# Kernel optimization log

Measured on AMD Instinct MI355X. Metric: run time of the kernel, lower is better.

Reference implementation:

```python
import jax, jax.numpy as jnp
import numpy as np

CONF_TH = 0.6      # confidence_threshold
IOU_TH = 0.45      # iou_threshold
MAX_WH = 4096.0    # class offset for class-aware NMS (agnostic=False)
TOP_K = 1024       # fixed candidate cap (analog of max_nms, jit-static)
MAX_DET = 300      # max detections per image
NC = 80
AGNOSTIC = False


def setup_inputs() -> dict:
    key = jax.random.key(0)
    k1, k2 = jax.random.split(key)
    prediction = jax.random.uniform(k1, (16, 25200, 85), dtype=jnp.float32)
    logits = jax.random.uniform(k2, (16, 25200, 80), dtype=jnp.float32)
    return {"prediction": prediction, "logits": logits}


def xywh2xyxy(b):
    cx, cy, w, h = b[:, 0], b[:, 1], b[:, 2], b[:, 3]
    return jnp.stack([cx - w * 0.5, cy - h * 0.5, cx + w * 0.5, cy + h * 0.5], axis=-1)


def box_iou(a, b):
    # a: [K,4], b: [K,4] in xyxy -> [K,K] IoU
    area_a = (a[:, 2] - a[:, 0]) * (a[:, 3] - a[:, 1])
    area_b = (b[:, 2] - b[:, 0]) * (b[:, 3] - b[:, 1])
    lt = jnp.maximum(a[:, None, :2], b[None, :, :2])
    rb = jnp.minimum(a[:, None, 2:], b[None, :, 2:])
    wh = jnp.clip(rb - lt, 0.0)
    inter = wh[..., 0] * wh[..., 1]
    return inter / (area_a[:, None] + area_b[None, :] - inter + 1e-9)


def _greedy_keep(iou, valid):
    # iou: [K,K] on score-descending boxes; valid: [K] bool
    K = iou.shape[0]
    ar = jnp.arange(K)

    def step(suppressed, i):
        keep_i = valid[i] & ~suppressed[i]
        suppressed = suppressed | (keep_i & (iou[i] > IOU_TH) & (ar > i))
        return suppressed, keep_i

    _, keep = jax.lax.scan(step, jnp.zeros((K,), dtype=bool), ar)
    return keep


def _nms_image(pred, logit):
    # pred: [N, 5+nc], logit: [N, nc]
    obj = pred[:, 4]
    cls_scores = pred[:, 5:] * obj[:, None]          # x[:,5:] *= x[:,4:5]
    conf = jnp.max(cls_scores, axis=-1)              # best-class confidence
    cls = jnp.argmax(cls_scores, axis=-1)
    valid = (obj > CONF_TH) & (conf > CONF_TH)       # xc gate + conf gate
    box = xywh2xyxy(pred[:, :4])

    score = jnp.where(valid, conf, -1.0)
    top_scores, idx = jax.lax.top_k(score, TOP_K)    # descending-score candidates
    box_k = box[idx]                                  # [K,4] original boxes
    cls_k = cls[idx]
    logit_k = logit[idx]
    valid_k = top_scores > CONF_TH

    # class-aware offset (agnostic=False) for NMS only
    off = 0.0 if AGNOSTIC else MAX_WH
    nms_boxes = box_k + cls_k[:, None].astype(box_k.dtype) * off

    iou = box_iou(nms_boxes, nms_boxes)
    keep = _greedy_keep(iou, valid_k)

    kept_score = jnp.where(keep, top_scores, -1.0)
    sel_score, sel = jax.lax.top_k(kept_score, MAX_DET)
    out_valid = sel_score > CONF_TH

    det = jnp.concatenate(
        [box_k[sel], top_scores[sel][:, None], cls_k[sel][:, None].astype(jnp.float32)],
        axis=1,
    )  # [max_det, 6] = [xyxy, conf, cls]
    det = jnp.where(out_valid[:, None], det, 0.0)
    logits_out = jnp.where(out_valid[:, None], logit_k[sel], 0.0)  # [max_det, nc]
    return det, out_valid, logits_out


def reference(prediction, logits):
    det, valid, logits_out = jax.vmap(_nms_image)(prediction, logits)
    return det, valid, logits_out
```

## Files before the change

kernel.cpp:

```cpp
#include <hip/hip_runtime.h>
#include <stdint.h>

#define CONF_THR 0.6f
#define IOU_THR  0.45f
#define MAX_WH_F 4096.0f
#define TOPK     1024
#define MAX_DET  300
#define NCLS     80
#define ROW      85
#define APB      128
#define RING     16

typedef unsigned int u32;
typedef unsigned long long u64;

__device__ __forceinline__ u32 f2s(float f) {
    u32 b = __float_as_uint(f);
    return b ^ ((u32)((int)b >> 31) | 0x80000000u);
}
__device__ __forceinline__ float s2f(u32 k) {
    u32 b = (k & 0x80000000u) ? (k ^ 0x80000000u) : ~k;
    return __uint_as_float(b);
}

__global__ __launch_bounds__(256) void k_score(const float* __restrict__ pred,
        u32* __restrict__ key, u32* __restrict__ cls, int NA) {
#pragma clang fp contract(off)
    int img = blockIdx.y;
    int a0 = blockIdx.x * APB;
    int count = min(APB, NA - a0);
    if (count <= 0) return;
    size_t baseoff = ((size_t)img * NA + a0) * ROW;
    const float* base = pred + baseoff;
    __shared__ __align__(16) float tile[APB * ROW];
    int nfloat = count * ROW;
    if ((baseoff & 3) == 0) {
        int nvec = nfloat >> 2;
        const float4* b4 = (const float4*)base;
        float4* t4 = (float4*)tile;
        for (int i = threadIdx.x; i < nvec; i += blockDim.x) t4[i] = b4[i];
        for (int i = (nvec << 2) + threadIdx.x; i < nfloat; i += blockDim.x)
            tile[i] = base[i];
    } else {
        for (int i = threadIdx.x; i < nfloat; i += blockDim.x) tile[i] = base[i];
    }
    __syncthreads();
    int t = threadIdx.x;
    if (t < count) {
        const float* r = tile + t * ROW;
        float obj = r[4];
        float maxv = -1.0f; int cl = 0;
        for (int j = 0; j < NCLS; ++j) {
            float v = r[5 + j] * obj;
            if (v > maxv) { maxv = v; cl = j; }
        }
        bool valid = (obj > CONF_THR) && (maxv > CONF_THR);
        float score = valid ? maxv : -1.0f;
        size_t g = (size_t)img * NA + a0 + t;
        key[g] = f2s(score);
        cls[g] = (u32)cl;
    }
}

__global__ __launch_bounds__(1024) void k_topk(const u32* __restrict__ key,
        const float* __restrict__ pred, const u32* __restrict__ cls,
        u32* __restrict__ top_idx, float* __restrict__ top_score,
        float* __restrict__ boxk, float* __restrict__ nmsbox,
        float* __restrict__ clsf, int NA) {
#pragma clang fp contract(off)
    int img = blockIdx.x;
    const u32* kb = key + (size_t)img * NA;
    __shared__ u32 whist[16 * 256];
    __shared__ u32 hfin[256];
    __shared__ int sh_d;
    __shared__ u32 sh_t;
    __shared__ u32 gcnt;
    __shared__ u64 skey[TOPK];
    int tid = threadIdx.x;
    int wid = tid >> 6, lane = tid & 63;
    u64 lanemask = (1ull << lane) - 1ull;
    u32 prefix = 0, target = TOPK;
    for (int level = 0; level < 4; ++level) {
        int shift = 24 - 8 * level;
        for (int i = tid; i < 16 * 256; i += 1024) whist[i] = 0;
        __syncthreads();
        for (int idx0 = 0; idx0 < NA; idx0 += 1024) {
            int idx = idx0 + tid;
            bool inb = idx < NA;
            u32 k = inb ? kb[idx] : 0u;
            bool in = inb && ((level == 0) || ((k >> (shift + 8)) == prefix));
            u32 d = (k >> shift) & 0xFFu;
            if (level == 0) {
                u64 peers = __ballot(in);
#pragma unroll
                for (int bit = 0; bit < 8; ++bit) {
                    u64 bb = __ballot((d >> bit) & 1u);
                    peers &= ((d >> bit) & 1u) ? bb : ~bb;
                }
                if (in) {
                    int leader = (int)(__ffsll((long long)peers) - 1);
                    if (lane == leader)
                        atomicAdd(&whist[(wid << 8) | d], (u32)__popcll(peers));
                }
            } else {
                if (in) atomicAdd(&whist[(wid << 8) | d], 1u);
            }
        }
        __syncthreads();
        if (tid < 256) {
            u32 s = 0;
#pragma unroll
            for (int w = 0; w < 16; ++w) s += whist[(w << 8) | tid];
            hfin[tid] = s;
        }
        __syncthreads();
        if (tid < 64) {
            u32 h0 = hfin[4 * tid], h1 = hfin[4 * tid + 1];
            u32 h2 = hfin[4 * tid + 2], h3 = hfin[4 * tid + 3];
            u32 s = h0 + h1 + h2 + h3;
            u32 t = s;
#pragma unroll
            for (int off = 1; off < 64; off <<= 1) {
                u32 o = (u32)__shfl_down((int)t, off);
                if (tid + off < 64) t += o;
            }
            u32 S0 = t, S1 = t - h0, S2 = S1 - h1, S3 = S2 - h2, S4 = t - s;
            u32 tg = target;
            if (S0 >= tg && S1 < tg) { sh_d = 4 * tid;     sh_t = tg - S1; }
            if (S1 >= tg && S2 < tg) { sh_d = 4 * tid + 1; sh_t = tg - S2; }
            if (S2 >= tg && S3 < tg) { sh_d = 4 * tid + 2; sh_t = tg - S3; }
            if (S3 >= tg && S4 < tg) { sh_d = 4 * tid + 3; sh_t = tg - S4; }
        }
        __syncthreads();
        prefix = (prefix << 8) | (u32)sh_d;
        target = sh_t;
    }
    u32 cutv = prefix;
    u32 R = target;
    u32 T = hfin[cutv & 0xFFu];
    if (tid == 0) gcnt = 0;
    __syncthreads();
    bool takeTies = (T == R);
    for (int c0 = 0; c0 < NA; c0 += 1024) {
        int idx = c0 + tid;
        bool inb = idx < NA;
        u32 k = inb ? kb[idx] : 0u;
        bool put = inb && ((k > cutv) || (takeTies && k == cutv));
        u64 ball = __ballot(put);
        if (ball) {
            int leader = (int)(__ffsll((long long)ball) - 1);
            u32 base = 0;
            if (lane == leader) base = atomicAdd(&gcnt, (u32)__popcll(ball));
            base = __shfl(base, leader);
            if (put)
                skey[base + (u32)__popcll(ball & lanemask)] =
                    ((u64)k << 32) | (u64)(u32)(NA - 1 - idx);
        }
    }
    __syncthreads();
    if (!takeTies) {
        u32 G = gcnt;
        if (tid < 64) {
            u32 cnt = 0;
            for (int c0 = 0; c0 < NA; c0 += 64) {
                int idx = c0 + tid;
                bool ist = (idx < NA) && (kb[idx] == cutv);
                u64 ball = __ballot(ist);
                u32 rank = cnt + (u32)__popcll(ball & lanemask);
                if (ist && rank < R)
                    skey[G + rank] = ((u64)cutv << 32) | (u64)(u32)(NA - 1 - idx);
                cnt += (u32)__popcll(ball);
                if (cnt >= R) break;
            }
        }
        __syncthreads();
    }
    int jprev = 0;
    for (int k2 = 2; k2 <= TOPK; k2 <<= 1) {
        for (int j = k2 >> 1; j > 0; j >>= 1) {
            if (j >= 64 || jprev >= 64) __syncthreads();
            int i = tid, ixj = i ^ j;
            if (ixj > i) {
                u64 a = skey[i], b = skey[ixj];
                bool desc = ((i & k2) == 0);
                if ((a < b) == desc) { skey[i] = b; skey[ixj] = a; }
            }
            jprev = j;
        }
    }
    __syncthreads();
    u64 kk = skey[tid];
    u32 aidx = (u32)(NA - 1) - (u32)(kk & 0xFFFFFFFFull);
    float sc = s2f((u32)(kk >> 32));
    int g = img * TOPK + tid;
    top_idx[g] = aidx;
    top_score[g] = sc;
    const float* r = pred + ((size_t)img * NA + aidx) * ROW;
    float cx = r[0], cy = r[1], w4 = r[2], h4 = r[3];
    float hw = w4 * 0.5f, hh = h4 * 0.5f;
    float x1 = cx - hw, y1 = cy - hh, x2 = cx + hw, y2 = cy + hh;
    u32 c = cls[(size_t)img * NA + aidx];
    float off = (float)c * MAX_WH_F;
    boxk[g * 4 + 0] = x1; boxk[g * 4 + 1] = y1;
    boxk[g * 4 + 2] = x2; boxk[g * 4 + 3] = y2;
    nmsbox[g * 4 + 0] = x1 + off; nmsbox[g * 4 + 1] = y1 + off;
    nmsbox[g * 4 + 2] = x2 + off; nmsbox[g * 4 + 3] = y2 + off;
    clsf[g] = (float)c;
}

__global__ __launch_bounds__(1024) void k_mask(const float* __restrict__ nmsbox,
        u64* __restrict__ mask) {
#pragma clang fp contract(off)
    int img = blockIdx.y;
    __shared__ float bx[TOPK + 32], by[TOPK + 32], bX[TOPK + 32], bY[TOPK + 32], ar[TOPK + 32];
    int tid = threadIdx.x;
    {
        const float4* nb = (const float4*)(nmsbox + (size_t)img * TOPK * 4);
        float4 b = nb[tid];
        int pi = tid + (tid >> 5);
        bx[pi] = b.x; by[pi] = b.y; bX[pi] = b.z; bY[pi] = b.w;
        ar[pi] = (b.z - b.x) * (b.w - b.y);
    }
    __syncthreads();
    int i = blockIdx.x * 64 + (tid >> 4);
    int w = tid & 15;
    int pi = i + (i >> 5);
    float ax = bx[pi], ay = by[pi], aX = bX[pi], aY = bY[pi], aa = ar[pi];
    u64 bits = 0;
    for (int jj = 0; jj < 64; ++jj) {
        int j = (w << 6) + jj;
        if (j > i) {
            int pj = j + (j >> 5);
            float ltx = fmaxf(ax, bx[pj]);
            float lty = fmaxf(ay, by[pj]);
            float rbx = fminf(aX, bX[pj]);
            float rby = fminf(aY, bY[pj]);
            float ww = fmaxf(rbx - ltx, 0.0f);
            float hh = fmaxf(rby - lty, 0.0f);
            float inter = ww * hh;
            float denom = ((aa + ar[pj]) - inter) + 1e-9f;
            float iou = inter / denom;
            if (iou > IOU_THR) bits |= (1ull << jj);
        }
    }
    mask[((size_t)img * TOPK + i) * 16 + w] = bits;
}

__global__ __launch_bounds__(1024) void k_nms(const u64* __restrict__ mask,
        const float* __restrict__ top_score,
        u32* __restrict__ sel, u32* __restrict__ selcnt, u32* __restrict__ dummy) {
    __shared__ u32 s_nvalid;
    __shared__ u64 keepw[16];
    int img = blockIdx.x;
    int tid = threadIdx.x;
    int lane = tid & 63;
    if (tid == 0) s_nvalid = 0;
    if (tid < 16) keepw[tid] = 0;
    __syncthreads();
    {
        float s = top_score[img * TOPK + tid];
        u64 b = __ballot(s > CONF_THR);
        if (lane == 0) atomicAdd(&s_nvalid, (u32)__popcll(b));
    }
    __syncthreads();
    const u64* mrow = mask + (size_t)img * TOPK * 16;
    if (tid >= 64) {
        const uint4* m16 = (const uint4*)mrow;
        u32 acc = 0;
        for (int i = tid - 64; i < 8192; i += 960) {
            uint4 v = m16[i];
            acc ^= v.x ^ v.y ^ v.z ^ v.w;
        }
        if (acc == 0xDEADBEEFu) *dummy = acc;
        return;
    }
    int nvalid = (int)s_nvalid;
    bool ld = lane < 16;
    u64 rem = 0;
    u64 pf[RING];
#pragma unroll
    for (int k = 0; k < RING; ++k)
        pf[k] = ld ? mrow[(size_t)k * 16 + lane] : 0ull;
    int nblk = (nvalid + 63) >> 6;
    int kept_total = 0;
    for (int blk = 0; blk < nblk; ++blk) {
        u64 kw = 0;
        int base = blk << 6;
#pragma unroll 16
        for (int t = 0; t < 64; ++t) {
            int i = base + t;
            u64 roww = pf[i & (RING - 1)];
            int nx = i + RING;
            pf[i & (RING - 1)] = (ld && nx < TOPK) ? mrow[(size_t)nx * 16 + lane] : 0ull;
            bool notsup = (lane == (i >> 6)) && !((rem >> (i & 63)) & 1ull);
            if (__ballot(notsup) != 0ull) {
                rem |= roww;
                kw |= (1ull << t);
            }
        }
        int over = nvalid - base;
        if (over < 64) kw &= (over <= 0) ? 0ull : ((1ull << over) - 1ull);
        if (lane == 0) keepw[blk] = kw;
        kept_total += (int)__popcll(kw);
        if (kept_total >= MAX_DET) break;
    }
    if (lane < 16) {
        u64 kw = keepw[lane];
        u32 rank = 0;
        for (int m = 0; m < 16; ++m)
            if (m < lane) rank += (u32)__popcll(keepw[m]);
        while (kw) {
            int b = (int)__ffsll((long long)kw) - 1;
            if (rank < MAX_DET) sel[img * MAX_DET + rank] = (u32)((lane << 6) + b);
            ++rank;
            kw &= kw - 1;
        }
    }
    if (lane == 0) selcnt[img] = (u32)min(kept_total, MAX_DET);
}

__global__ void k_out(const float* __restrict__ logits,
        const u32* __restrict__ top_idx, const float* __restrict__ top_score,
        const float* __restrict__ boxk, const float* __restrict__ clsf,
        const u32* __restrict__ sel, const u32* __restrict__ selcnt,
        float* __restrict__ out, int NA, int B) {
    int img = blockIdx.y;
    int t = blockIdx.x;
    int tid = threadIdx.x;
    u32 K = selcnt[img];
    size_t detoff = ((size_t)img * MAX_DET + t) * 6;
    size_t voff = (size_t)B * MAX_DET * 6 + (size_t)img * MAX_DET + t;
    size_t loff = (size_t)B * MAX_DET * 7 + ((size_t)img * MAX_DET + t) * NCLS;
    if ((u32)t < K) {
        int slot = (int)sel[img * MAX_DET + t];
        int g = img * TOPK + slot;
        u32 aidx = top_idx[g];
        if (tid < NCLS)      out[loff + tid] = logits[((size_t)img * NA + aidx) * NCLS + tid];
        else if (tid < 84)   out[detoff + (tid - 80)] = boxk[(size_t)g * 4 + (tid - 80)];
        else if (tid == 84)  out[detoff + 4] = top_score[g];
        else if (tid == 85)  out[detoff + 5] = clsf[g];
        else if (tid == 86)  out[voff] = 1.0f;
    } else {
        if (tid < NCLS)      out[loff + tid] = 0.0f;
        else if (tid < 86)   out[detoff + (tid - 80)] = 0.0f;
        else if (tid == 86)  out[voff] = 0.0f;
    }
}

extern "C" void kernel_launch(void* const* d_in, const int* in_sizes, int n_in,
                              void* d_out, int out_size, void* d_ws, size_t ws_size,
                              hipStream_t stream) {
    const float* pred = (const float*)d_in[0];
    const float* logits = (const float*)d_in[1];
    float* out = (float*)d_out;
    const int B = out_size / (MAX_DET * (6 + 1 + NCLS));
    const int NA = in_sizes[0] / (B * ROW);

    char* p = (char*)d_ws;
    auto alloc = [&](size_t bytes) -> void* {
        void* r = (void*)p;
        p += (bytes + 255) & ~(size_t)255;
        return r;
    };
    u32* key       = (u32*)alloc((size_t)B * NA * 4);
    u32* cls       = (u32*)alloc((size_t)B * NA * 4);
    u32* top_idx   = (u32*)alloc((size_t)B * TOPK * 4);
    float* top_scr = (float*)alloc((size_t)B * TOPK * 4);
    float* boxk    = (float*)alloc((size_t)B * TOPK * 16);
    float* nmsbox  = (float*)alloc((size_t)B * TOPK * 16);
    float* clsf    = (float*)alloc((size_t)B * TOPK * 4);
    u64* mask      = (u64*)alloc((size_t)B * TOPK * 16 * 8);
    u32* sel       = (u32*)alloc((size_t)B * MAX_DET * 4);
    u32* selcnt    = (u32*)alloc((size_t)(B + 1) * 4);
    u32* dummy     = selcnt + B;

    k_score<<<dim3((NA + APB - 1) / APB, B), 256, 0, stream>>>(pred, key, cls, NA);
    k_topk<<<dim3(B), 1024, 0, stream>>>(key, pred, cls, top_idx, top_scr,
                                         boxk, nmsbox, clsf, NA);
    k_mask<<<dim3(TOPK / 64, B), 1024, 0, stream>>>(nmsbox, mask);
    k_nms<<<dim3(B), 1024, 0, stream>>>(mask, top_scr, sel, selcnt, dummy);
    k_out<<<dim3(MAX_DET, B), 128, 0, stream>>>(logits, top_idx, top_scr, boxk, clsf,
                                                sel, selcnt, out, NA, B);
}
```

Baseline: 368.1 us.

## Cache 16-bit keys in LDS, compact candidates for top-k, fuse output into NMS

```diff
diff --git a/kernel.cpp b/kernel.cpp
--- a/kernel.cpp
+++ b/kernel.cpp
@@ -10,6 +10,7 @@
 #define ROW      85
 #define APB      128
 #define RING     16
+#define CAND2    1024
 
 typedef unsigned int u32;
 typedef unsigned long long u64;
@@ -21,6 +22,39 @@
 __device__ __forceinline__ float s2f(u32 k) {
     u32 b = (k & 0x80000000u) ? (k ^ 0x80000000u) : ~k;
     return __uint_as_float(b);
+}
+
+__device__ __forceinline__ void hist_add(u32* hist, u32 d, bool in, int lane) {
+    u64 peers = __ballot(in);
+#pragma unroll
+    for (int bit = 0; bit < 8; ++bit) {
+        u64 bb = __ballot((d >> bit) & 1u);
+        peers &= ((d >> bit) & 1u) ? bb : ~bb;
+    }
+    if (in) {
+        int leader = (int)(__ffsll((long long)peers) - 1);
+        if (lane == leader) atomicAdd(&hist[d], (u32)__popcll(peers));
+    }
+}
+
+__device__ __forceinline__ void suffix_select(const u32* hist, int tid, u32 target,
+                                              int* sh_d, u32* sh_t) {
+    if (tid < 64) {
+        u32 h0 = hist[4 * tid], h1 = hist[4 * tid + 1];
+        u32 h2 = hist[4 * tid + 2], h3 = hist[4 * tid + 3];
+        u32 s = h0 + h1 + h2 + h3;
+        u32 t = s;
+#pragma unroll
+        for (int off = 1; off < 64; off <<= 1) {
+            u32 o = (u32)__shfl_down((int)t, off);
+            if (tid + off < 64) t += o;
+        }
+        u32 S0 = t, S1 = t - h0, S2 = S1 - h1, S3 = S2 - h2, S4 = t - s;
+        if (S0 >= target && S1 < target) { *sh_d = 4 * tid;     *sh_t = target - S1; }
+        if (S1 >= target && S2 < target) { *sh_d = 4 * tid + 1; *sh_t = target - S2; }
+        if (S2 >= target && S3 < target) { *sh_d = 4 * tid + 2; *sh_t = target - S3; }
+        if (S3 >= target && S4 < target) { *sh_d = 4 * tid + 3; *sh_t = target - S4; }
+    }
 }
 
 __global__ __launch_bounds__(256) void k_score(const float* __restrict__ pred,
@@ -70,74 +104,94 @@
 #pragma clang fp contract(off)
     int img = blockIdx.x;
     const u32* kb = key + (size_t)img * NA;
-    __shared__ u32 whist[16 * 256];
-    __shared__ u32 hfin[256];
+    __shared__ u32 hist[256];
     __shared__ int sh_d;
     __shared__ u32 sh_t;
-    __shared__ u32 gcnt;
-    __shared__ u64 skey[TOPK];
+    __shared__ u32 gcnt, ccnt;
+    struct ShA { unsigned short key16[25216]; u32 cand2[CAND2]; };
+    union ShU { ShA a; u64 skey[TOPK]; };
+    __shared__ ShU sh;
     int tid = threadIdx.x;
-    int wid = tid >> 6, lane = tid & 63;
+    int lane = tid & 63;
     u64 lanemask = (1ull << lane) - 1ull;
-    u32 prefix = 0, target = TOPK;
-    for (int level = 0; level < 4; ++level) {
+    u32 target = TOPK;
+
+    if (tid < 256) hist[tid] = 0;
+    __syncthreads();
+    for (int c0 = 0; c0 < NA; c0 += 1024) {
+        int idx = c0 + tid;
+        bool inb = idx < NA;
+        u32 k = inb ? kb[idx] : 0u;
+        if (inb) sh.a.key16[idx] = (unsigned short)(k >> 16);
+        hist_add(hist, k >> 24, inb, lane);
+    }
+    __syncthreads();
+    suffix_select(hist, tid, target, &sh_d, &sh_t);
+    __syncthreads();
+    u32 d0 = (u32)sh_d; target = sh_t;
+
+    if (tid < 256) hist[tid] = 0;
+    __syncthreads();
+    for (int c0 = 0; c0 < NA; c0 += 1024) {
+        int idx = c0 + tid;
+        bool inb = idx < NA;
+        u32 v = inb ? (u32)sh.a.key16[idx] : 0u;
+        bool in = inb && ((v >> 8) == d0);
+        hist_add(hist, v & 0xFFu, in, lane);
+    }
+    __syncthreads();
+    suffix_select(hist, tid, target, &sh_d, &sh_t);
+    __syncthreads();
+    u32 prefix = (d0 << 8) | (u32)sh_d;
+    target = sh_t;
+
+    if (tid == 0) ccnt = 0;
+    __syncthreads();
+    for (int c0 = 0; c0 < NA; c0 += 1024) {
+        int idx = c0 + tid;
+        bool inb = idx < NA;
+        u32 k = inb ? kb[idx] : 0u;
+        bool put = inb && ((k >> 16) == prefix);
+        u64 ball = __ballot(put);
+        if (ball) {
+            int leader = (int)(__ffsll((long long)ball) - 1);
+            u32 base = 0;
+            if (lane == leader) base = atomicAdd(&ccnt, (u32)__popcll(ball));
+            base = __shfl(base, leader);
+            u32 pos = base + (u32)__popcll(ball & lanemask);
+            if (put && pos < CAND2) sh.a.cand2[pos] = k;
+        }
+    }
+    __syncthreads();
+    u32 nc = ccnt;
+
+    for (int level = 2; level < 4; ++level) {
         int shift = 24 - 8 * level;
-        for (int i = tid; i < 16 * 256; i += 1024) whist[i] = 0;
+        if (tid < 256) hist[tid] = 0;
         __syncthreads();
-        for (int idx0 = 0; idx0 < NA; idx0 += 1024) {
-            int idx = idx0 + tid;
-            bool inb = idx < NA;
-            u32 k = inb ? kb[idx] : 0u;
-            bool in = inb && ((level == 0) || ((k >> (shift + 8)) == prefix));
-            u32 d = (k >> shift) & 0xFFu;
-            if (level == 0) {
-                u64 peers = __ballot(in);
-#pragma unroll
-                for (int bit = 0; bit < 8; ++bit) {
-                    u64 bb = __ballot((d >> bit) & 1u);
-                    peers &= ((d >> bit) & 1u) ? bb : ~bb;
-                }
-                if (in) {
-                    int leader = (int)(__ffsll((long long)peers) - 1);
-                    if (lane == leader)
-                        atomicAdd(&whist[(wid << 8) | d], (u32)__popcll(peers));
-                }
-            } else {
-                if (in) atomicAdd(&whist[(wid << 8) | d], 1u);
+        if (nc <= CAND2) {
+            u32 k = (tid < (int)nc) ? sh.a.cand2[tid] : 0u;
+            bool in = (tid < (int)nc) &&
+                      ((level == 2) || ((k >> (shift + 8)) == prefix));
+            hist_add(hist, (k >> shift) & 0xFFu, in, lane);
+        } else {
+            for (int c0 = 0; c0 < NA; c0 += 1024) {
+                int idx = c0 + tid;
+                bool inb = idx < NA;
+                u32 k = inb ? kb[idx] : 0u;
+                bool in = inb && ((k >> (shift + 8)) == prefix);
+                hist_add(hist, (k >> shift) & 0xFFu, in, lane);
             }
         }
         __syncthreads();
-        if (tid < 256) {
-            u32 s = 0;
-#pragma unroll
-            for (int w = 0; w < 16; ++w) s += whist[(w << 8) | tid];
-            hfin[tid] = s;
-        }
-        __syncthreads();
-        if (tid < 64) {
-            u32 h0 = hfin[4 * tid], h1 = hfin[4 * tid + 1];
-            u32 h2 = hfin[4 * tid + 2], h3 = hfin[4 * tid + 3];
-            u32 s = h0 + h1 + h2 + h3;
-            u32 t = s;
-#pragma unroll
-            for (int off = 1; off < 64; off <<= 1) {
-                u32 o = (u32)__shfl_down((int)t, off);
-                if (tid + off < 64) t += o;
-            }
-            u32 S0 = t, S1 = t - h0, S2 = S1 - h1, S3 = S2 - h2, S4 = t - s;
-            u32 tg = target;
-            if (S0 >= tg && S1 < tg) { sh_d = 4 * tid;     sh_t = tg - S1; }
-            if (S1 >= tg && S2 < tg) { sh_d = 4 * tid + 1; sh_t = tg - S2; }
-            if (S2 >= tg && S3 < tg) { sh_d = 4 * tid + 2; sh_t = tg - S3; }
-            if (S3 >= tg && S4 < tg) { sh_d = 4 * tid + 3; sh_t = tg - S4; }
-        }
+        suffix_select(hist, tid, target, &sh_d, &sh_t);
         __syncthreads();
         prefix = (prefix << 8) | (u32)sh_d;
         target = sh_t;
     }
     u32 cutv = prefix;
     u32 R = target;
-    u32 T = hfin[cutv & 0xFFu];
+    u32 T = hist[cutv & 0xFFu];
     if (tid == 0) gcnt = 0;
     __syncthreads();
     bool takeTies = (T == R);
@@ -153,7 +207,7 @@
             if (lane == leader) base = atomicAdd(&gcnt, (u32)__popcll(ball));
             base = __shfl(base, leader);
             if (put)
-                skey[base + (u32)__popcll(ball & lanemask)] =
+                sh.skey[base + (u32)__popcll(ball & lanemask)] =
                     ((u64)k << 32) | (u64)(u32)(NA - 1 - idx);
         }
     }
@@ -168,7 +222,7 @@
                 u64 ball = __ballot(ist);
                 u32 rank = cnt + (u32)__popcll(ball & lanemask);
                 if (ist && rank < R)
-                    skey[G + rank] = ((u64)cutv << 32) | (u64)(u32)(NA - 1 - idx);
+                    sh.skey[G + rank] = ((u64)cutv << 32) | (u64)(u32)(NA - 1 - idx);
                 cnt += (u32)__popcll(ball);
                 if (cnt >= R) break;
             }
@@ -181,15 +235,15 @@
             if (j >= 64 || jprev >= 64) __syncthreads();
             int i = tid, ixj = i ^ j;
             if (ixj > i) {
-                u64 a = skey[i], b = skey[ixj];
+                u64 a = sh.skey[i], b = sh.skey[ixj];
                 bool desc = ((i & k2) == 0);
-                if ((a < b) == desc) { skey[i] = b; skey[ixj] = a; }
+                if ((a < b) == desc) { sh.skey[i] = b; sh.skey[ixj] = a; }
             }
             jprev = j;
         }
     }
     __syncthreads();
-    u64 kk = skey[tid];
+    u64 kk = sh.skey[tid];
     u32 aidx = (u32)(NA - 1) - (u32)(kk & 0xFFFFFFFFull);
     float sc = s2f((u32)(kk >> 32));
     int g = img * TOPK + tid;
@@ -247,12 +301,17 @@
 }
 
 __global__ __launch_bounds__(1024) void k_nms(const u64* __restrict__ mask,
-        const float* __restrict__ top_score,
-        u32* __restrict__ sel, u32* __restrict__ selcnt, u32* __restrict__ dummy) {
+        const float* __restrict__ top_score, const u32* __restrict__ top_idx,
+        const float* __restrict__ boxk, const float* __restrict__ clsf,
+        const float* __restrict__ logits, float* __restrict__ out,
+        u32* __restrict__ dummy, int NA, int B) {
     __shared__ u32 s_nvalid;
     __shared__ u64 keepw[16];
+    __shared__ u32 s_sel[MAX_DET];
+    __shared__ u32 s_cnt;
     int img = blockIdx.x;
     int tid = threadIdx.x;
+    int wid = tid >> 6;
     int lane = tid & 63;
     if (tid == 0) s_nvalid = 0;
     if (tid < 16) keepw[tid] = 0;
@@ -272,78 +331,69 @@
             acc ^= v.x ^ v.y ^ v.z ^ v.w;
         }
         if (acc == 0xDEADBEEFu) *dummy = acc;
-        return;
-    }
-    int nvalid = (int)s_nvalid;
-    bool ld = lane < 16;
-    u64 rem = 0;
-    u64 pf[RING];
+    } else {
+        int nvalid = (int)s_nvalid;
+        bool ld = lane < 16;
+        u64 rem = 0;
+        u64 pf[RING];
 #pragma unroll
-    for (int k = 0; k < RING; ++k)
-        pf[k] = ld ? mrow[(size_t)k * 16 + lane] : 0ull;
-    int nblk = (nvalid + 63) >> 6;
-    int kept_total = 0;
-    for (int blk = 0; blk < nblk; ++blk) {
-        u64 kw = 0;
-        int base = blk << 6;
+        for (int k = 0; k < RING; ++k)
+            pf[k] = ld ? mrow[(size_t)k * 16 + lane] : 0ull;
+        int nblk = (nvalid + 63) >> 6;
+        int kept_total = 0;
+        for (int blk = 0; blk < nblk; ++blk) {
+            u64 kw = 0;
+            int base = blk << 6;
 #pragma unroll 16
-        for (int t = 0; t < 64; ++t) {
-            int i = base + t;
-            u64 roww = pf[i & (RING - 1)];
-            int nx = i + RING;
-            pf[i & (RING - 1)] = (ld && nx < TOPK) ? mrow[(size_t)nx * 16 + lane] : 0ull;
-            bool notsup = (lane == (i >> 6)) && !((rem >> (i & 63)) & 1ull);
-            if (__ballot(notsup) != 0ull) {
-                rem |= roww;
-                kw |= (1ull << t);
+            for (int t = 0; t < 64; ++t) {
+                int i = base + t;
+                u64 roww = pf[i & (RING - 1)];
+                int nx = i + RING;
+                pf[i & (RING - 1)] = (ld && nx < TOPK) ? mrow[(size_t)nx * 16 + lane] : 0ull;
+                bool notsup = (lane == (i >> 6)) && !((rem >> (i & 63)) & 1ull);
+                if (__ballot(notsup) != 0ull) {
+                    rem |= roww;
+                    kw |= (1ull << t);
+                }
             }
-        }
-        int over = nvalid - base;
-        if (over < 64) kw &= (over <= 0) ? 0ull : ((1ull << over) - 1ull);
-        if (lane == 0) keepw[blk] = kw;
-        kept_total += (int)__popcll(kw);
-        if (kept_total >= MAX_DET) break;
-    }
-    if (lane < 16) {
-        u64 kw = keepw[lane];
-        u32 rank = 0;
-        for (int m = 0; m < 16; ++m)
-            if (m < lane) rank += (u32)__popcll(keepw[m]);
-        while (kw) {
-            int b = (int)__ffsll((long long)kw) - 1;
-            if (rank < MAX_DET) sel[img * MAX_DET + rank] = (u32)((lane << 6) + b);
-            ++rank;
-            kw &= kw - 1;
-        }
-    }
-    if (lane == 0) selcnt[img] = (u32)min(kept_total, MAX_DET);
-}
-
-__global__ void k_out(const float* __restrict__ logits,
-        const u32* __restrict__ top_idx, const float* __restrict__ top_score,
-        const float* __restrict__ boxk, const float* __restrict__ clsf,
-        const u32* __restrict__ sel, const u32* __restrict__ selcnt,
-        float* __restrict__ out, int NA, int B) {
-    int img = blockIdx.y;
-    int t = blockIdx.x;
-    int tid = threadIdx.x;
-    u32 K = selcnt[img];
-    size_t detoff = ((size_t)img * MAX_DET + t) * 6;
-    size_t voff = (size_t)B * MAX_DET * 6 + (size_t)img * MAX_DET + t;
-    size_t loff = (size_t)B * MAX_DET * 7 + ((size_t)img * MAX_DET + t) * NCLS;
-    if ((u32)t < K) {
-        int slot = (int)sel[img * MAX_DET + t];
+            int over = nvalid - base;
+            if (over < 64) kw &= (over <= 0) ? 0ull : ((1ull << over) - 1ull);
+            if (lane == 0) keepw[blk] = kw;
+            kept_total += (int)__popcll(kw);
+            if (kept_total >= MAX_DET) break;
+        }
+        if (lane < 16) {
+            u64 kw = keepw[lane];
+            u32 rank = 0;
+            for (int m = 0; m < 16; ++m)
+                if (m < lane) rank += (u32)__popcll(keepw[m]);
+            while (kw) {
+                int b = (int)__ffsll((long long)kw) - 1;
+                if (rank < MAX_DET) s_sel[rank] = (u32)((lane << 6) + b);
+                ++rank;
+                kw &= kw - 1;
+            }
+        }
+        if (lane == 0) s_cnt = (u32)min(kept_total, MAX_DET);
+    }
+    __syncthreads();
+    u32 K = s_cnt;
+    for (int t = wid; t < MAX_DET; t += 16) {
+        bool v = (u32)t < K;
+        int slot = v ? (int)s_sel[t] : 0;
         int g = img * TOPK + slot;
         u32 aidx = top_idx[g];
-        if (tid < NCLS)      out[loff + tid] = logits[((size_t)img * NA + aidx) * NCLS + tid];
-        else if (tid < 84)   out[detoff + (tid - 80)] = boxk[(size_t)g * 4 + (tid - 80)];
-        else if (tid == 84)  out[detoff + 4] = top_score[g];
-        else if (tid == 85)  out[detoff + 5] = clsf[g];
-        else if (tid == 86)  out[voff] = 1.0f;
-    } else {
-        if (tid < NCLS)      out[loff + tid] = 0.0f;
-        else if (tid < 86)   out[detoff + (tid - 80)] = 0.0f;
-        else if (tid == 86)  out[voff] = 0.0f;
+        size_t detoff = ((size_t)img * MAX_DET + t) * 6;
+        size_t voff = (size_t)B * MAX_DET * 6 + (size_t)img * MAX_DET + t;
+        size_t loff = (size_t)B * MAX_DET * 7 + ((size_t)img * MAX_DET + t) * NCLS;
+        const float* lrow = logits + ((size_t)img * NA + aidx) * NCLS;
+        out[loff + lane] = v ? lrow[lane] : 0.0f;
+        int l2 = lane + 64;
+        if (lane < 16)       out[loff + l2] = v ? lrow[l2] : 0.0f;
+        else if (lane < 20)  out[detoff + (lane - 16)] = v ? boxk[(size_t)g * 4 + (lane - 16)] : 0.0f;
+        else if (lane == 20) out[detoff + 4] = v ? top_score[g] : 0.0f;
+        else if (lane == 21) out[detoff + 5] = v ? clsf[g] : 0.0f;
+        else if (lane == 22) out[voff] = v ? 1.0f : 0.0f;
     }
 }
 
@@ -370,15 +420,12 @@
     float* nmsbox  = (float*)alloc((size_t)B * TOPK * 16);
     float* clsf    = (float*)alloc((size_t)B * TOPK * 4);
     u64* mask      = (u64*)alloc((size_t)B * TOPK * 16 * 8);
-    u32* sel       = (u32*)alloc((size_t)B * MAX_DET * 4);
-    u32* selcnt    = (u32*)alloc((size_t)(B + 1) * 4);
-    u32* dummy     = selcnt + B;
+    u32* dummy     = (u32*)alloc(256);
 
     k_score<<<dim3((NA + APB - 1) / APB, B), 256, 0, stream>>>(pred, key, cls, NA);
     k_topk<<<dim3(B), 1024, 0, stream>>>(key, pred, cls, top_idx, top_scr,
                                          boxk, nmsbox, clsf, NA);
     k_mask<<<dim3(TOPK / 64, B), 1024, 0, stream>>>(nmsbox, mask);
-    k_nms<<<dim3(B), 1024, 0, stream>>>(mask, top_scr, sel, selcnt, dummy);
-    k_out<<<dim3(MAX_DET, B), 128, 0, stream>>>(logits, top_idx, top_scr, boxk, clsf,
-                                                sel, selcnt, out, NA, B);
-}
+    k_nms<<<dim3(B), 1024, 0, stream>>>(mask, top_scr, top_idx, boxk, clsf,
+                                        logits, out, dummy, NA, B);
+}
```

Result: slower. 408.5 us (+11.0%).
